# Kernel tuning notes

Hardware: AMD Instinct MI355X
Metric: run time of the kernel (lower is better)

The kernel has to match this reference:

```python
import jax, jax.numpy as jnp
import numpy as np

B, N, C = 8, 1024, 768
NUM_HEADS = 12
HEAD_DIM = C // NUM_HEADS  # 64
WS = 32                    # window_size[0] == window_size[1] == H == W
REL_DIM = 2 * WS - 1       # 63


def setup_inputs() -> dict:
    key = jax.random.key(0)
    ks = jax.random.split(key, 7)
    x = jax.random.normal(ks[0], (B, N, C), dtype=jnp.float32)
    qkv_w = jax.random.normal(ks[1], (3 * C, C), dtype=jnp.float32) * 0.02
    qkv_b = jnp.zeros((3 * C,), dtype=jnp.float32)
    proj_w = jax.random.normal(ks[2], (C, C), dtype=jnp.float32) * 0.02
    proj_b = jnp.zeros((C,), dtype=jnp.float32)
    rel_pos_h = jax.random.normal(ks[3], (REL_DIM, HEAD_DIM), dtype=jnp.float32) * 0.02
    rel_pos_w = jax.random.normal(ks[4], (REL_DIM, HEAD_DIM), dtype=jnp.float32) * 0.02
    return {
        "x": x,
        "qkv_w": qkv_w,
        "qkv_b": qkv_b,
        "proj_w": proj_w,
        "proj_b": proj_b,
        "rel_pos_h": rel_pos_h,
        "rel_pos_w": rel_pos_w,
        "H": WS,
        "W": WS,
    }


def reference(x, qkv_w, qkv_b, proj_w, proj_b, rel_pos_h, rel_pos_w, H, W):
    B_, N_, C_ = x.shape
    heads = NUM_HEADS
    hd = C_ // heads
    scale = hd ** -0.5

    # qkv projection: (B, N, 3, heads, hd) -> (3, B, heads, N, hd)
    qkv = (x @ qkv_w.T + qkv_b).reshape(B_, N_, 3, heads, hd).transpose(2, 0, 3, 1, 4)
    q, k, v = qkv[0], qkv[1], qkv[2]
    q = q * scale

    # raw scores (B, heads, N, N)
    attn = jnp.einsum('bhqd,bhkd->bhqk', q, k)

    # decomposed relative position bias (q_shape == k_shape -> ratios are 1.0)
    dist_h = jnp.arange(H)[:, None] - jnp.arange(H)[None, :] + (H - 1)
    dist_w = jnp.arange(W)[:, None] - jnp.arange(W)[None, :] + (W - 1)
    Rh = rel_pos_h[dist_h]  # (H, H, hd)
    Rw = rel_pos_w[dist_w]  # (W, W, hd)

    r_q = q.reshape(B_, heads, H, W, hd)
    rel_h = jnp.einsum('byhwc,hkc->byhwk', r_q, Rh)  # (B, heads, H, W, k_h)
    rel_w = jnp.einsum('byhwc,wkc->byhwk', r_q, Rw)  # (B, heads, H, W, k_w)

    attn = (attn.reshape(B_, heads, H, W, H, W)
            + rel_h[:, :, :, :, :, None]
            + rel_w[:, :, :, :, None, :]).reshape(B_, heads, N_, N_)

    attn = jax.nn.softmax(attn, axis=-1)
    out = jnp.einsum('bhqk,bhkd->bhqd', attn, v)
    out = out.transpose(0, 2, 1, 3).reshape(B_, N_, heads * hd)
    return out @ proj_w.T + proj_b
```

## Files before the change

### kernel.cpp

```cpp
#include <hip/hip_runtime.h>
#include <cstddef>

typedef short s4v __attribute__((ext_vector_type(4)));
typedef short s8v __attribute__((ext_vector_type(8)));
typedef float f4v __attribute__((ext_vector_type(4)));

__device__ __forceinline__ unsigned short f2bf(float f) {
    union { float f; unsigned u; } v; v.f = f;
    unsigned r = v.u + 0x7fff + ((v.u >> 16) & 1);
    return (unsigned short)(r >> 16);
}
__device__ __forceinline__ float bf2f(unsigned short u) {
    union { unsigned u; float f; } v; v.u = ((unsigned)u) << 16;
    return v.f;
}

__device__ __forceinline__ void gl_lds16(const void* g, void* l) {
    __builtin_amdgcn_global_load_lds(
        (const __attribute__((address_space(1))) void*)g,
        (__attribute__((address_space(3))) void*)l, 16, 0, 0);
}

#define QSC   0.18033688011112043f
#define EOFF  23.082320654223414f

__global__ __launch_bounds__(256) void to_bf16_all(
    const float* __restrict__ x, const float* __restrict__ qw,
    const float* __restrict__ pw, unsigned short* __restrict__ xd,
    unsigned short* __restrict__ qd, unsigned short* __restrict__ pd)
{
    int i = blockIdx.x * 256 + threadIdx.x;
    const float* s; unsigned short* d; int j;
    if (i < 786432)       { s = x;  d = xd; j = i; }
    else if (i < 1007616) { s = qw; d = qd; j = i - 786432; }
    else                  { s = pw; d = pd; j = i - 1007616; }
    float4 f0 = ((const float4*)s)[j * 2];
    float4 f1 = ((const float4*)s)[j * 2 + 1];
    uint4 pk;
    pk.x = (unsigned)f2bf(f0.x) | ((unsigned)f2bf(f0.y) << 16);
    pk.y = (unsigned)f2bf(f0.z) | ((unsigned)f2bf(f0.w) << 16);
    pk.z = (unsigned)f2bf(f1.x) | ((unsigned)f2bf(f1.y) << 16);
    pk.w = (unsigned)f2bf(f1.z) | ((unsigned)f2bf(f1.w) << 16);
    ((uint4*)d)[j] = pk;
}

__global__ __launch_bounds__(256) void qkv_gemm_mfma(
    const unsigned short* __restrict__ A, const unsigned short* __restrict__ W,
    const float* __restrict__ bias,
    unsigned short* __restrict__ qb, unsigned short* __restrict__ kb,
    unsigned short* __restrict__ vt)
{
    __shared__ __align__(16) unsigned short As[128 * 32];
    __shared__ __align__(16) unsigned short Bs[128 * 32];
    const int t     = threadIdx.x;
    const int bc    = blockIdx.x;
    const int br    = blockIdx.y;
    const int wv    = t >> 6;
    const int lane  = t & 63;
    const int col16 = lane & 15;
    const int quad  = lane >> 4;
    const int w4    = lane >> 2;
    const int k8    = (lane & 3) << 3;
    const int mw    = wv >> 1, nw = wv & 1;

    const unsigned short* Ag = A + (size_t)(br * 128 + (wv << 5) + w4) * 768 + k8;
    const unsigned short* Wg = W + (size_t)(bc * 128 + (wv << 5) + w4) * 768 + k8;
    unsigned short* Asw = &As[(wv << 5) * 32];
    unsigned short* Bsw = &Bs[(wv << 5) * 32];

    f4v acc[4][4];
#pragma unroll
    for (int mt = 0; mt < 4; ++mt)
#pragma unroll
        for (int nt = 0; nt < 4; ++nt) {
            acc[mt][nt][0] = 0.f; acc[mt][nt][1] = 0.f;
            acc[mt][nt][2] = 0.f; acc[mt][nt][3] = 0.f;
        }

    for (int k0 = 0; k0 < 768; k0 += 32) {
        __syncthreads();
        gl_lds16(Ag + k0,             Asw);
        gl_lds16(Ag + k0 + 16 * 768,  Asw + 16 * 32);
        gl_lds16(Wg + k0,             Bsw);
        gl_lds16(Wg + k0 + 16 * 768,  Bsw + 16 * 32);
        __syncthreads();

        s8v a[4], b[4];
#pragma unroll
        for (int mt = 0; mt < 4; ++mt)
            a[mt] = *(const s8v*)&As[(mw * 64 + mt * 16 + col16) * 32 + quad * 8];
#pragma unroll
        for (int nt = 0; nt < 4; ++nt)
            b[nt] = *(const s8v*)&Bs[(nw * 64 + nt * 16 + col16) * 32 + quad * 8];
#pragma unroll
        for (int mt = 0; mt < 4; ++mt)
#pragma unroll
            for (int nt = 0; nt < 4; ++nt)
                acc[mt][nt] = __builtin_amdgcn_mfma_f32_16x16x32_bf16(
                    a[mt], b[nt], acc[mt][nt], 0, 0, 0);
    }

    const int which = bc / 6;
    const int cb    = (bc % 6) * 128 + nw * 64;
    const int m0    = br * 128 + mw * 64 + quad * 4;
    if (which == 2) {
#pragma unroll
        for (int nt = 0; nt < 4; ++nt) {
            int c    = cb + nt * 16 + col16;
            int head = c >> 6, d = c & 63;
            float bv = bias[1536 + c];
#pragma unroll
            for (int mt = 0; mt < 4; ++mt) {
                int mb  = m0 + mt * 16;
                int bbk = mb >> 10, tok = mb & 1023;
                uint2 pk;
                pk.x = (unsigned)f2bf(acc[mt][nt][0] + bv)
                     | ((unsigned)f2bf(acc[mt][nt][1] + bv) << 16);
                pk.y = (unsigned)f2bf(acc[mt][nt][2] + bv)
                     | ((unsigned)f2bf(acc[mt][nt][3] + bv) << 16);
                *(uint2*)&vt[((size_t)(bbk * 12 + head)) * 65536 + (size_t)d * 1024 + tok] = pk;
            }
        }
    } else {
        const float sc = (which == 0) ? QSC : 1.0f;
        unsigned short* dst = (which == 0) ? qb : kb;
#pragma unroll
        for (int nt = 0; nt < 4; ++nt) {
            int c    = cb + nt * 16 + col16;
            int head = c >> 6, d = c & 63;
            float bv = bias[which * 768 + c];
#pragma unroll
            for (int mt = 0; mt < 4; ++mt) {
#pragma unroll
                for (int i = 0; i < 4; ++i) {
                    int m   = m0 + mt * 16 + i;
                    int bbk = m >> 10, tok = m & 1023;
                    dst[(((size_t)(bbk * 12 + head) << 10) + tok) * 64 + d] =
                        f2bf((acc[mt][nt][i] + bv) * sc);
                }
            }
        }
    }
}

__global__ __launch_bounds__(256) void proj_gemm_mfma(
    const unsigned short* __restrict__ A, const unsigned short* __restrict__ W,
    const float* __restrict__ bias, float* __restrict__ Out)
{
    __shared__ __align__(16) unsigned short As[128 * 32];
    __shared__ __align__(16) unsigned short Bs[128 * 32];
    const int t     = threadIdx.x;
    const int bc    = blockIdx.x;
    const int br    = blockIdx.y;
    const int wv    = t >> 6;
    const int lane  = t & 63;
    const int col16 = lane & 15;
    const int quad  = lane >> 4;
    const int w4    = lane >> 2;
    const int k8    = (lane & 3) << 3;
    const int mw    = wv >> 1, nw = wv & 1;

    const unsigned short* Ag = A + (size_t)(br * 128 + (wv << 5) + w4) * 768 + k8;
    const unsigned short* Wg = W + (size_t)(bc * 128 + (wv << 5) + w4) * 768 + k8;
    unsigned short* Asw = &As[(wv << 5) * 32];
    unsigned short* Bsw = &Bs[(wv << 5) * 32];

    f4v acc[4][4];
#pragma unroll
    for (int mt = 0; mt < 4; ++mt)
#pragma unroll
        for (int nt = 0; nt < 4; ++nt) {
            acc[mt][nt][0] = 0.f; acc[mt][nt][1] = 0.f;
            acc[mt][nt][2] = 0.f; acc[mt][nt][3] = 0.f;
        }

    for (int k0 = 0; k0 < 768; k0 += 32) {
        __syncthreads();
        gl_lds16(Ag + k0,             Asw);
        gl_lds16(Ag + k0 + 16 * 768,  Asw + 16 * 32);
        gl_lds16(Wg + k0,             Bsw);
        gl_lds16(Wg + k0 + 16 * 768,  Bsw + 16 * 32);
        __syncthreads();

        s8v a[4], b[4];
#pragma unroll
        for (int mt = 0; mt < 4; ++mt)
            a[mt] = *(const s8v*)&As[(mw * 64 + mt * 16 + col16) * 32 + quad * 8];
#pragma unroll
        for (int nt = 0; nt < 4; ++nt)
            b[nt] = *(const s8v*)&Bs[(nw * 64 + nt * 16 + col16) * 32 + quad * 8];
#pragma unroll
        for (int mt = 0; mt < 4; ++mt)
#pragma unroll
            for (int nt = 0; nt < 4; ++nt)
                acc[mt][nt] = __builtin_amdgcn_mfma_f32_16x16x32_bf16(
                    a[mt], b[nt], acc[mt][nt], 0, 0, 0);
    }

    const int m0 = br * 128 + mw * 64 + quad * 4;
#pragma unroll
    for (int nt = 0; nt < 4; ++nt) {
        int c    = bc * 128 + nw * 64 + nt * 16 + col16;
        float bv = bias[c];
#pragma unroll
        for (int mt = 0; mt < 4; ++mt) {
#pragma unroll
            for (int i = 0; i < 4; ++i) {
                int m = m0 + mt * 16 + i;
                Out[(size_t)m * 768 + c] = acc[mt][nt][i] + bv;
            }
        }
    }
}

__global__ __launch_bounds__(256) void bias_prep_mfma(
    const unsigned short* __restrict__ Q, const float* __restrict__ Rh,
    const float* __restrict__ Rw, unsigned short* __restrict__ qhb,
    unsigned short* __restrict__ qwb)
{
    __shared__ __align__(16) char smem[36864];
    unsigned short (*Qs)[72]  = (unsigned short (*)[72])smem;
    unsigned short (*Rs)[72]  = (unsigned short (*)[72])(smem + 18432);
    unsigned short (*Wsm)[72] = (unsigned short (*)[72])(smem + 27648);
    float (*G)[66]            = (float (*)[66])smem;

    const int t    = threadIdx.x;
    const int tc8  = blockIdx.x;
    const int bh   = blockIdx.y;
    const int tok0 = tc8 << 7;

    for (int id = t; id < 1024; id += 256) {
        int row = id >> 3, g8 = (id & 7) << 3;
        *(uint4*)&Qs[row][g8] =
            *(const uint4*)(Q + ((size_t)bh * 1024 + tok0 + row) * 64 + g8);
    }
    for (int id = t; id < 512; id += 256) {
        int row = id >> 3, g8 = (id & 7) << 3;
        unsigned short* dh = &Rs[row][g8];
        unsigned short* dw = &Wsm[row][g8];
        if (row < 63) {
            const float* sh = Rh + row * 64 + g8;
            const float* sw = Rw + row * 64 + g8;
            float4 a = *(const float4*)sh; float4 b = *(const float4*)(sh + 4);
            float4 c = *(const float4*)sw; float4 d = *(const float4*)(sw + 4);
            dh[0] = f2bf(a.x); dh[1] = f2bf(a.y); dh[2] = f2bf(a.z); dh[3] = f2bf(a.w);
            dh[4] = f2bf(b.x); dh[5] = f2bf(b.y); dh[6] = f2bf(b.z); dh[7] = f2bf(b.w);
            dw[0] = f2bf(c.x); dw[1] = f2bf(c.y); dw[2] = f2bf(c.z); dw[3] = f2bf(c.w);
            dw[4] = f2bf(d.x); dw[5] = f2bf(d.y); dw[6] = f2bf(d.z); dw[7] = f2bf(d.w);
        } else {
#pragma unroll
            for (int j = 0; j < 8; ++j) { dh[j] = 0; dw[j] = 0; }
        }
    }
    __syncthreads();

    const int wv    = t >> 6;
    const int lane  = t & 63;
    const int col16 = lane & 15;
    const int quad  = lane >> 4;
    const int r0    = wv << 5;

    s8v qa[2][2], rb[4][2], wb[4][2];
#pragma unroll
    for (int mt = 0; mt < 2; ++mt)
#pragma unroll
        for (int kc = 0; kc < 2; ++kc)
            qa[mt][kc] = *(const s8v*)&Qs[r0 + mt * 16 + col16][kc * 32 + quad * 8];
#pragma unroll
    for (int nt = 0; nt < 4; ++nt)
#pragma unroll
        for (int kc = 0; kc < 2; ++kc) {
            rb[nt][kc] = *(const s8v*)&Rs[nt * 16 + col16][kc * 32 + quad * 8];
            wb[nt][kc] = *(const s8v*)&Wsm[nt * 16 + col16][kc * 32 + quad * 8];
        }

    f4v ah[2][4], aw[2][4];
#pragma unroll
    for (int mt = 0; mt < 2; ++mt)
#pragma unroll
        for (int nt = 0; nt < 4; ++nt) {
            f4v z; z[0] = 0.f; z[1] = 0.f; z[2] = 0.f; z[3] = 0.f;
            ah[mt][nt] = z; aw[mt][nt] = z;
        }
#pragma unroll
    for (int mt = 0; mt < 2; ++mt)
#pragma unroll
        for (int nt = 0; nt < 4; ++nt) {
            ah[mt][nt] = __builtin_amdgcn_mfma_f32_16x16x32_bf16(qa[mt][0], rb[nt][0], ah[mt][nt], 0, 0, 0);
            ah[mt][nt] = __builtin_amdgcn_mfma_f32_16x16x32_bf16(qa[mt][1], rb[nt][1], ah[mt][nt], 0, 0, 0);
            aw[mt][nt] = __builtin_amdgcn_mfma_f32_16x16x32_bf16(qa[mt][0], wb[nt][0], aw[mt][nt], 0, 0, 0);
            aw[mt][nt] = __builtin_amdgcn_mfma_f32_16x16x32_bf16(qa[mt][1], wb[nt][1], aw[mt][nt], 0, 0, 0);
        }
    __syncthreads();

#pragma unroll
    for (int mt = 0; mt < 2; ++mt)
#pragma unroll
        for (int nt = 0; nt < 4; ++nt)
#pragma unroll
            for (int i = 0; i < 4; ++i)
                G[r0 + mt * 16 + quad * 4 + i][nt * 16 + col16] = ah[mt][nt][i];
    __syncthreads();
    for (int id = t; id < 2048; id += 256) {
        int tok = id >> 4, c2 = (id & 15) << 1;
        int i_img = (tc8 << 2) + (tok >> 5);
        float g0 = G[tok][i_img - c2 + 31];
        float g1 = G[tok][i_img - c2 + 30];
        unsigned pk = (unsigned)f2bf(g0) | ((unsigned)f2bf(g1) << 16);
        *(unsigned*)&qhb[(((size_t)bh << 10) + tok0 + tok) * 32 + c2] = pk;
    }
    __syncthreads();

#pragma unroll
    for (int mt = 0; mt < 2; ++mt)
#pragma unroll
        for (int nt = 0; nt < 4; ++nt)
#pragma unroll
            for (int i = 0; i < 4; ++i)
                G[r0 + mt * 16 + quad * 4 + i][nt * 16 + col16] = aw[mt][nt][i];
    __syncthreads();
    for (int id = t; id < 2048; id += 256) {
        int tok = id >> 4, c2 = (id & 15) << 1;
        int j = tok & 31;
        float g0 = G[tok][j - c2 + 31];
        float g1 = G[tok][j - c2 + 30];
        unsigned pk = (unsigned)f2bf(g0) | ((unsigned)f2bf(g1) << 16);
        *(unsigned*)&qwb[(((size_t)bh << 10) + tok0 + tok) * 32 + c2] = pk;
    }
}

__global__ __launch_bounds__(256, 4) void attn_mfma(
    const unsigned short* __restrict__ Q, const unsigned short* __restrict__ K,
    const unsigned short* __restrict__ Vt,
    const unsigned short* __restrict__ qhb, const unsigned short* __restrict__ qwb,
    unsigned short* __restrict__ Out)
{
    const int t  = threadIdx.x;
    const int id  = blockIdx.x;
    const int xcd = id & 7;
    const int wq  = id >> 3;
    const int bh  = xcd * 12 + (wq % 12);
    const int qt2 = wq / 12;
    const int b   = bh / 12;
    const int h   = bh - b * 12;
    const int q0  = qt2 << 6;

    __shared__ __align__(16) unsigned short Ks[64 * 72];
    __shared__ __align__(16) unsigned short Vs[64 * 72];
    __shared__ float qh_s[64][33];

    const unsigned short* Kp = K  + (size_t)bh * 65536;
    const unsigned short* Vp = Vt + (size_t)bh * 65536;

    {
        const unsigned* qhp = (const unsigned*)(qhb + ((size_t)bh * 1024 + q0) * 32);
        for (int i2 = t; i2 < 1024; i2 += 256) {
            int row = i2 >> 4, c2 = (i2 & 15) << 1;
            unsigned ph = qhp[i2];
            qh_s[row][c2]     = bf2f((unsigned short)(ph & 0xffff)) - EOFF;
            qh_s[row][c2 + 1] = bf2f((unsigned short)(ph >> 16))    - EOFF;
        }
    }

    const int wv = t >> 6;
    const int lane = t & 63;
    const int c  = lane & 15;
    const int qd = lane >> 4;

    s8v qf0, qf1;
    float uw[8];
    {
        const size_t row = (size_t)bh * 1024 + q0 + (wv << 4) + c;
        const unsigned short* qp = Q + row * 64 + qd * 8;
        qf0 = *(const s8v*)qp;
        qf1 = *(const s8v*)(qp + 32);
        s8v w8 = *(const s8v*)(qwb + row * 32 + qd * 8);
#pragma unroll
        for (int j = 0; j < 8; ++j) uw[j] = bf2f((unsigned short)w8[j]);
    }

    const int e0 = t * 8, e1 = t * 8 + 2048;
    const int g0 = e0 >> 6, g1 = e1 >> 6, s0 = e0 & 63, s1 = e1 & 63;
    const int L0 = (g0 & 32) | ((g0 & 4) << 2) | ((g0 & 24) >> 1) | (g0 & 3);
    const int L1 = (g1 & 32) | ((g1 & 4) << 2) | ((g1 & 24) >> 1) | (g1 & 3);
    {
        uint4 pk0 = *(const uint4*)(Kp + e0);
        uint4 pk1 = *(const uint4*)(Kp + e1);
        uint4 pv0 = *(const uint4*)(Vp + (size_t)g0 * 1024 + s0);
        uint4 pv1 = *(const uint4*)(Vp + (size_t)g1 * 1024 + s1);
        *(uint4*)&Ks[L0 * 72 + s0] = pk0;
        *(uint4*)&Ks[L1 * 72 + s1] = pk1;
        *(uint4*)&Vs[g0 * 72 + s0] = pv0;
        *(uint4*)&Vs[g1 * 72 + s1] = pv1;
    }
    __syncthreads();

    f4v o[4];
#pragma unroll
    for (int dt = 0; dt < 4; ++dt) { o[dt][0] = 0.f; o[dt][1] = 0.f; o[dt][2] = 0.f; o[dt][3] = 0.f; }
    float lp = 0.f;

    for (int kt = 0; kt < 16; ++kt) {
        uint4 pk0, pk1, pv0, pv1;
        if (kt < 15) {
            const int k0n = (kt + 1) << 6;
            pk0 = *(const uint4*)(Kp + (size_t)k0n * 64 + e0);
            pk1 = *(const uint4*)(Kp + (size_t)k0n * 64 + e1);
            pv0 = *(const uint4*)(Vp + (size_t)g0 * 1024 + k0n + s0);
            pv1 = *(const uint4*)(Vp + (size_t)g1 * 1024 + k0n + s1);
        }

        f4v sc[4];
#pragma unroll
        for (int T = 0; T < 4; ++T) {
            s8v lo = *(const s8v*)&Ks[(T * 16 + c) * 72 + qd * 8];
            s8v hi = *(const s8v*)&Ks[(T * 16 + c) * 72 + 32 + qd * 8];
            f4v z; z[0] = 0.f; z[1] = 0.f; z[2] = 0.f; z[3] = 0.f;
            z = __builtin_amdgcn_mfma_f32_16x16x32_bf16(lo, qf0, z, 0, 0, 0);
            z = __builtin_amdgcn_mfma_f32_16x16x32_bf16(hi, qf1, z, 0, 0, 0);
            sc[T] = z;
        }

        const float qhv0 = qh_s[(wv << 4) + c][(kt << 1)];
        const float qhv1 = qh_s[(wv << 4) + c][(kt << 1) + 1];

        s8v pa0, pa1;
#pragma unroll
        for (int j = 0; j < 4; ++j) {
            float pe = __builtin_amdgcn_exp2f(sc[0][j] + qhv0 + uw[j]);
            lp += pe; pa0[j] = (short)f2bf(pe);
        }
#pragma unroll
        for (int j = 0; j < 4; ++j) {
            float pe = __builtin_amdgcn_exp2f(sc[1][j] + qhv0 + uw[4 + j]);
            lp += pe; pa0[4 + j] = (short)f2bf(pe);
        }
#pragma unroll
        for (int j = 0; j < 4; ++j) {
            float pe = __builtin_amdgcn_exp2f(sc[2][j] + qhv1 + uw[j]);
            lp += pe; pa1[j] = (short)f2bf(pe);
        }
#pragma unroll
        for (int j = 0; j < 4; ++j) {
            float pe = __builtin_amdgcn_exp2f(sc[3][j] + qhv1 + uw[4 + j]);
            lp += pe; pa1[4 + j] = (short)f2bf(pe);
        }

#pragma unroll
        for (int dt = 0; dt < 4; ++dt) {
            s8v vlo = *(const s8v*)&Vs[(dt * 16 + c) * 72 + qd * 8];
            s8v vhi = *(const s8v*)&Vs[(dt * 16 + c) * 72 + 32 + qd * 8];
            o[dt] = __builtin_amdgcn_mfma_f32_16x16x32_bf16(pa0, vlo, o[dt], 0, 0, 0);
            o[dt] = __builtin_amdgcn_mfma_f32_16x16x32_bf16(pa1, vhi, o[dt], 0, 0, 0);
        }

        __syncthreads();
        if (kt < 15) {
            *(uint4*)&Ks[L0 * 72 + s0] = pk0;
            *(uint4*)&Ks[L1 * 72 + s1] = pk1;
            *(uint4*)&Vs[g0 * 72 + s0] = pv0;
            *(uint4*)&Vs[g1 * 72 + s1] = pv1;
        }
        __syncthreads();
    }

    lp += __shfl_xor(lp, 16);
    lp += __shfl_xor(lp, 32);

#pragma unroll
    for (int i = 0; i < 4; ++i) {
        float inv = 1.f / __shfl(lp, (qd << 2) + i);
        int qr = q0 + (wv << 4) + (qd << 2) + i;
        unsigned short* dst = Out + ((size_t)b * 1024 + qr) * 768 + h * 64;
#pragma unroll
        for (int dt = 0; dt < 4; ++dt)
            dst[dt * 16 + c] = f2bf(o[dt][i] * inv);
    }
}

extern "C" void kernel_launch(void* const* d_in, const int* in_sizes, int n_in,
                              void* d_out, int out_size, void* d_ws, size_t ws_size,
                              hipStream_t stream) {
    const float* x      = (const float*)d_in[0];
    const float* qkv_w  = (const float*)d_in[1];
    const float* qkv_b  = (const float*)d_in[2];
    const float* proj_w = (const float*)d_in[3];
    const float* proj_b = (const float*)d_in[4];
    const float* rel_h  = (const float*)d_in[5];
    const float* rel_w  = (const float*)d_in[6];
    float* out = (float*)d_out;

    char* ws = (char*)d_ws;
    unsigned short* qbuf  = (unsigned short*)(ws);
    unsigned short* kbuf  = (unsigned short*)(ws + 12582912);
    unsigned short* vtbuf = (unsigned short*)(ws + 25165824);
    unsigned short* xab   = (unsigned short*)(ws + 37748736);
    unsigned short* wqb   = (unsigned short*)(ws + 50331648);
    unsigned short* wpb   = (unsigned short*)(ws + 53870592);
    unsigned short* qhb   = (unsigned short*)(ws + 55050240);
    unsigned short* qwb   = (unsigned short*)(ws + 61341696);

    to_bf16_all<<<4224, 256, 0, stream>>>(x, qkv_w, proj_w, xab, wqb, wpb);
    qkv_gemm_mfma<<<dim3(18, 64), 256, 0, stream>>>(xab, wqb, qkv_b, qbuf, kbuf, vtbuf);
    bias_prep_mfma<<<dim3(8, 96), 256, 0, stream>>>(qbuf, rel_h, rel_w, qhb, qwb);
    attn_mfma<<<1536, 256, 0, stream>>>(qbuf, kbuf, vtbuf, qhb, qwb, xab);
    proj_gemm_mfma<<<dim3(6, 64), 256, 0, stream>>>(xab, wpb, proj_b, out);
}
```

Before: 226.1 us.

## Double-buffer LDS tiles and remap GEMM blocks for XCD locality

Both the QKV and output-projection GEMMs now use two LDS buffers. The next K-slice is issued with global_load_lds while MFMAs run on the current slice, which removes one barrier per iteration and hides some load latency. The 2D grid is flattened and remapped so that blocks landing on the same XCD share row tiles, aiming for better L2 reuse. In exchange the LDS footprint per block doubles, which may reduce occupancy.

```diff
diff --git a/kernel.cpp b/kernel.cpp
--- a/kernel.cpp
+++ b/kernel.cpp
@@ -50,11 +50,14 @@
     unsigned short* __restrict__ qb, unsigned short* __restrict__ kb,
     unsigned short* __restrict__ vt)
 {
-    __shared__ __align__(16) unsigned short As[128 * 32];
-    __shared__ __align__(16) unsigned short Bs[128 * 32];
+    __shared__ __align__(16) unsigned short As[2][128 * 32];
+    __shared__ __align__(16) unsigned short Bs[2][128 * 32];
     const int t     = threadIdx.x;
-    const int bc    = blockIdx.x;
-    const int br    = blockIdx.y;
+    const int lin   = blockIdx.x;
+    const int xcd   = lin & 7;
+    const int sq    = lin >> 3;
+    const int br    = (xcd << 3) + (sq & 7);
+    const int bc    = sq >> 3;
     const int wv    = t >> 6;
     const int lane  = t & 63;
     const int col16 = lane & 15;
@@ -65,8 +68,7 @@
 
     const unsigned short* Ag = A + (size_t)(br * 128 + (wv << 5) + w4) * 768 + k8;
     const unsigned short* Wg = W + (size_t)(bc * 128 + (wv << 5) + w4) * 768 + k8;
-    unsigned short* Asw = &As[(wv << 5) * 32];
-    unsigned short* Bsw = &Bs[(wv << 5) * 32];
+    const int wo = (wv << 5) * 32;
 
     f4v acc[4][4];
 #pragma unroll
@@ -77,21 +79,32 @@
             acc[mt][nt][2] = 0.f; acc[mt][nt][3] = 0.f;
         }
 
+    gl_lds16(Ag,            &As[0][wo]);
+    gl_lds16(Ag + 16 * 768, &As[0][wo + 16 * 32]);
+    gl_lds16(Wg,            &Bs[0][wo]);
+    gl_lds16(Wg + 16 * 768, &Bs[0][wo + 16 * 32]);
+
     for (int k0 = 0; k0 < 768; k0 += 32) {
         __syncthreads();
-        gl_lds16(Ag + k0,             Asw);
-        gl_lds16(Ag + k0 + 16 * 768,  Asw + 16 * 32);
-        gl_lds16(Wg + k0,             Bsw);
-        gl_lds16(Wg + k0 + 16 * 768,  Bsw + 16 * 32);
-        __syncthreads();
+        const int cur = (k0 >> 5) & 1;
+        if (k0 < 736) {
+            unsigned short* An = &As[cur ^ 1][wo];
+            unsigned short* Bn = &Bs[cur ^ 1][wo];
+            gl_lds16(Ag + k0 + 32,            An);
+            gl_lds16(Ag + k0 + 32 + 16 * 768, An + 16 * 32);
+            gl_lds16(Wg + k0 + 32,            Bn);
+            gl_lds16(Wg + k0 + 32 + 16 * 768, Bn + 16 * 32);
+        }
+        const unsigned short* Ab = As[cur];
+        const unsigned short* Bb = Bs[cur];
 
         s8v a[4], b[4];
 #pragma unroll
         for (int mt = 0; mt < 4; ++mt)
-            a[mt] = *(const s8v*)&As[(mw * 64 + mt * 16 + col16) * 32 + quad * 8];
+            a[mt] = *(const s8v*)&Ab[(mw * 64 + mt * 16 + col16) * 32 + quad * 8];
 #pragma unroll
         for (int nt = 0; nt < 4; ++nt)
-            b[nt] = *(const s8v*)&Bs[(nw * 64 + nt * 16 + col16) * 32 + quad * 8];
+            b[nt] = *(const s8v*)&Bb[(nw * 64 + nt * 16 + col16) * 32 + quad * 8];
 #pragma unroll
         for (int mt = 0; mt < 4; ++mt)
 #pragma unroll
@@ -147,11 +160,14 @@
     const unsigned short* __restrict__ A, const unsigned short* __restrict__ W,
     const float* __restrict__ bias, float* __restrict__ Out)
 {
-    __shared__ __align__(16) unsigned short As[128 * 32];
-    __shared__ __align__(16) unsigned short Bs[128 * 32];
+    __shared__ __align__(16) unsigned short As[2][128 * 32];
+    __shared__ __align__(16) unsigned short Bs[2][128 * 32];
     const int t     = threadIdx.x;
-    const int bc    = blockIdx.x;
-    const int br    = blockIdx.y;
+    const int lin   = blockIdx.x;
+    const int xcd   = lin & 7;
+    const int sq    = lin >> 3;
+    const int br    = (xcd << 3) + (sq & 7);
+    const int bc    = sq >> 3;
     const int wv    = t >> 6;
     const int lane  = t & 63;
     const int col16 = lane & 15;
@@ -162,8 +178,7 @@
 
     const unsigned short* Ag = A + (size_t)(br * 128 + (wv << 5) + w4) * 768 + k8;
     const unsigned short* Wg = W + (size_t)(bc * 128 + (wv << 5) + w4) * 768 + k8;
-    unsigned short* Asw = &As[(wv << 5) * 32];
-    unsigned short* Bsw = &Bs[(wv << 5) * 32];
+    const int wo = (wv << 5) * 32;
 
     f4v acc[4][4];
 #pragma unroll
@@ -174,21 +189,32 @@
             acc[mt][nt][2] = 0.f; acc[mt][nt][3] = 0.f;
         }
 
+    gl_lds16(Ag,            &As[0][wo]);
+    gl_lds16(Ag + 16 * 768, &As[0][wo + 16 * 32]);
+    gl_lds16(Wg,            &Bs[0][wo]);
+    gl_lds16(Wg + 16 * 768, &Bs[0][wo + 16 * 32]);
+
     for (int k0 = 0; k0 < 768; k0 += 32) {
         __syncthreads();
-        gl_lds16(Ag + k0,             Asw);
-        gl_lds16(Ag + k0 + 16 * 768,  Asw + 16 * 32);
-        gl_lds16(Wg + k0,             Bsw);
-        gl_lds16(Wg + k0 + 16 * 768,  Bsw + 16 * 32);
-        __syncthreads();
+        const int cur = (k0 >> 5) & 1;
+        if (k0 < 736) {
+            unsigned short* An = &As[cur ^ 1][wo];
+            unsigned short* Bn = &Bs[cur ^ 1][wo];
+            gl_lds16(Ag + k0 + 32,            An);
+            gl_lds16(Ag + k0 + 32 + 16 * 768, An + 16 * 32);
+            gl_lds16(Wg + k0 + 32,            Bn);
+            gl_lds16(Wg + k0 + 32 + 16 * 768, Bn + 16 * 32);
+        }
+        const unsigned short* Ab = As[cur];
+        const unsigned short* Bb = Bs[cur];
 
         s8v a[4], b[4];
 #pragma unroll
         for (int mt = 0; mt < 4; ++mt)
-            a[mt] = *(const s8v*)&As[(mw * 64 + mt * 16 + col16) * 32 + quad * 8];
+            a[mt] = *(const s8v*)&Ab[(mw * 64 + mt * 16 + col16) * 32 + quad * 8];
 #pragma unroll
         for (int nt = 0; nt < 4; ++nt)
-            b[nt] = *(const s8v*)&Bs[(nw * 64 + nt * 16 + col16) * 32 + quad * 8];
+            b[nt] = *(const s8v*)&Bb[(nw * 64 + nt * 16 + col16) * 32 + quad * 8];
 #pragma unroll
         for (int mt = 0; mt < 4; ++mt)
 #pragma unroll
@@ -501,8 +527,8 @@
     unsigned short* qwb   = (unsigned short*)(ws + 61341696);
 
     to_bf16_all<<<4224, 256, 0, stream>>>(x, qkv_w, proj_w, xab, wqb, wpb);
-    qkv_gemm_mfma<<<dim3(18, 64), 256, 0, stream>>>(xab, wqb, qkv_b, qbuf, kbuf, vtbuf);
+    qkv_gemm_mfma<<<1152, 256, 0, stream>>>(xab, wqb, qkv_b, qbuf, kbuf, vtbuf);
     bias_prep_mfma<<<dim3(8, 96), 256, 0, stream>>>(qbuf, rel_h, rel_w, qhb, qwb);
     attn_mfma<<<1536, 256, 0, stream>>>(qbuf, kbuf, vtbuf, qhb, qwb, xab);
-    proj_gemm_mfma<<<dim3(6, 64), 256, 0, stream>>>(xab, wpb, proj_b, out);
-}
+    proj_gemm_mfma<<<384, 256, 0, stream>>>(xab, wpb, proj_b, out);
+}
```

Result: no change. 226.6 us (+0.2%).
